# Optimization experiments

Hardware: AMD Instinct MI355X
Metric: run time of the kernel (lower is better)

## Reference

```python
import jax, jax.numpy as jnp
import numpy as np

B, N, D = 16, 4096, 64  # (batch*heads, seq_len, head_dim)

def setup_inputs() -> dict:
    key = jax.random.key(0)
    kq, kk, kv = jax.random.split(key, 3)
    queries = jax.random.normal(kq, (B, N, D), dtype=jnp.float32)
    keys = jax.random.normal(kk, (B, N, D), dtype=jnp.float32)
    values = jax.random.normal(kv, (B, N, D), dtype=jnp.float32)
    masking = jnp.zeros((B, N), dtype=jnp.float32)
    return {"queries": queries, "keys": keys, "values": values, "masking": masking}

def reference(queries, keys, values, masking):
    # Faithful to source: masks() computes the additive mask but returns
    # `inputs` unchanged (bug in original), so `masking` is a no-op.
    d = queries.shape[-1]
    scores = jnp.einsum('bnd,bmd->bnm', queries, keys) / jnp.sqrt(jnp.float32(d))
    attn = jax.nn.softmax(scores, axis=-1)
    # Dropout(rate=0) at inference is identity.
    out = jnp.einsum('bnm,bmd->bnd', attn, values)
    return out
```

## Files before the change

### kernel.cpp

```cpp
#include <hip/hip_runtime.h>
#include <hip/hip_bf16.h>

#define B_    16
#define N_    4096
#define D_    64
#define QBLK  128
#define KVBLK 64
#define KTILES (N_ / KVBLK)

typedef __attribute__((ext_vector_type(8))) short short8v;
typedef __attribute__((ext_vector_type(4))) float f32x4;
typedef __attribute__((ext_vector_type(4))) unsigned uint4v;

__device__ __forceinline__ short f2bf(float x) {
    union { float f; unsigned u; } c; c.f = x;
    unsigned r = c.u + 0x7FFFu + ((c.u >> 16) & 1u);
    return (short)(r >> 16);
}
__device__ __forceinline__ unsigned cvtpk(float lo, float hi) {
    unsigned r;
    asm("v_cvt_pk_bf16_f32 %0, %1, %2" : "=v"(r) : "v"(lo), "v"(hi));
    return r;
}
__device__ __forceinline__ float fexp2(float x) {
    float r;
    asm("v_exp_f32 %0, %1" : "=v"(r) : "v"(x));
    return r;
}

#define GLDS16(g, l)                                                      \
    __builtin_amdgcn_global_load_lds(                                     \
        (const __attribute__((address_space(1))) void*)(g),               \
        (__attribute__((address_space(3))) void*)(l), 16, 0, 0)

__global__ __launch_bounds__(256) void conv_k(const float* __restrict__ K,
                                              short* __restrict__ Kp) {
    const int idx  = blockIdx.x * 256 + threadIdx.x;
    const int nout = idx >> 3;
    const int c8   = (idx & 7) << 3;
    const int p    = nout & 63;
    const int sig  = (p & 3) | (((p >> 4) & 1) << 2) |
                     (((p >> 2) & 3) << 3) | ((p >> 5) << 5);
    const int nsrc = (nout & ~63) | sig;
    const float* src = K + (size_t)nsrc * D_ + c8;
    const f32x4 a = *(const f32x4*)src;
    const f32x4 b = *(const f32x4*)(src + 4);
    short8v o;
    o[0] = f2bf(a[0]); o[1] = f2bf(a[1]); o[2] = f2bf(a[2]); o[3] = f2bf(a[3]);
    o[4] = f2bf(b[0]); o[5] = f2bf(b[1]); o[6] = f2bf(b[2]); o[7] = f2bf(b[3]);
    const int cs = c8 ^ ((p & 7) << 3);
    *(short8v*)(Kp + (size_t)nout * D_ + cs) = o;
}

__global__ __launch_bounds__(256) void conv_v(const float* __restrict__ V,
                                              short* __restrict__ Vp) {
    __shared__ short Tl[64][68];
    const int b  = blockIdx.x >> 6;
    const int n0 = (blockIdx.x & 63) * 64;
    const int t  = threadIdx.x;
    const int r  = t >> 2;
    const int c0 = (t & 3) * 16;
    const float* src = V + ((size_t)b * N_ + n0 + r) * D_ + c0;
    const f32x4 v0 = *(const f32x4*)(src);
    const f32x4 v1 = *(const f32x4*)(src + 4);
    const f32x4 v2 = *(const f32x4*)(src + 8);
    const f32x4 v3 = *(const f32x4*)(src + 12);
    short8v lo, hi;
    lo[0]=f2bf(v0[0]); lo[1]=f2bf(v0[1]); lo[2]=f2bf(v0[2]); lo[3]=f2bf(v0[3]);
    lo[4]=f2bf(v1[0]); lo[5]=f2bf(v1[1]); lo[6]=f2bf(v1[2]); lo[7]=f2bf(v1[3]);
    hi[0]=f2bf(v2[0]); hi[1]=f2bf(v2[1]); hi[2]=f2bf(v2[2]); hi[3]=f2bf(v2[3]);
    hi[4]=f2bf(v3[0]); hi[5]=f2bf(v3[1]); hi[6]=f2bf(v3[2]); hi[7]=f2bf(v3[3]);
    *(short8v*)&Tl[r][c0]     = lo;
    *(short8v*)&Tl[r][c0 + 8] = hi;
    __syncthreads();
    const int d  = t >> 2;
    const int nb = (t & 3) * 16;
    const int s  = (d & 7) << 3;
    short8v o0, o1;
    #pragma unroll
    for (int j = 0; j < 8; ++j) {
        o0[j] = Tl[nb + j][d];
        o1[j] = Tl[nb + 8 + j][d];
    }
    short* dst = Vp + ((size_t)b * D_ + d) * N_ + n0;
    *(short8v*)(dst + (nb ^ s))       = o0;
    *(short8v*)(dst + ((nb + 8) ^ s)) = o1;
}

__global__ __launch_bounds__(256) void attn_fwd(
    const float* __restrict__ Qg, const short* __restrict__ Kp,
    const short* __restrict__ Vp, float* __restrict__ Og)
{
    __shared__ __align__(16) short Kl[4][KVBLK][D_];
    __shared__ __align__(16) short Vl[4][D_][KVBLK];

    const int tid  = threadIdx.x;
    const int w    = tid >> 6;
    const int lane = tid & 63;
    const int g    = lane >> 4;
    const int r16  = lane & 15;

    const int wg    = (blockIdx.x & 7) * 64 + (blockIdx.x >> 3);
    const int batch = wg >> 5;
    const int q0    = (wg & 31) * QBLK;

    const float SC = 0.18033688011112042f;
    const float* qrowA = Qg + ((size_t)batch * N_ + q0 + 32 * w + r16) * D_;
    const float* qrowB = qrowA + 16 * D_;
    short8v qfA[2], qfB[2];
    #pragma unroll
    for (int c = 0; c < 2; ++c) {
        const f32x4 a0 = *(const f32x4*)(qrowA + 32 * c + 8 * g);
        const f32x4 a1 = *(const f32x4*)(qrowA + 32 * c + 8 * g + 4);
        const f32x4 b0 = *(const f32x4*)(qrowB + 32 * c + 8 * g);
        const f32x4 b1 = *(const f32x4*)(qrowB + 32 * c + 8 * g + 4);
        short8v fa, fb;
        fa[0] = f2bf(a0[0] * SC); fa[1] = f2bf(a0[1] * SC);
        fa[2] = f2bf(a0[2] * SC); fa[3] = f2bf(a0[3] * SC);
        fa[4] = f2bf(a1[0] * SC); fa[5] = f2bf(a1[1] * SC);
        fa[6] = f2bf(a1[2] * SC); fa[7] = f2bf(a1[3] * SC);
        fb[0] = f2bf(b0[0] * SC); fb[1] = f2bf(b0[1] * SC);
        fb[2] = f2bf(b0[2] * SC); fb[3] = f2bf(b0[3] * SC);
        fb[4] = f2bf(b1[0] * SC); fb[5] = f2bf(b1[1] * SC);
        fb[6] = f2bf(b1[2] * SC); fb[7] = f2bf(b1[3] * SC);
        qfA[c] = fa;
        qfB[c] = fb;
    }

    f32x4 oA[4], oB[4];
    #pragma unroll
    for (int dt = 0; dt < 4; ++dt) {
        oA[dt] = (f32x4){0.f, 0.f, 0.f, 0.f};
        oB[dt] = (f32x4){0.f, 0.f, 0.f, 0.f};
    }
    float lA = 0.f, lB = 0.f;

    const short* kbase = Kp + (size_t)batch * N_ * D_;
    const short* vbase = Vp + (size_t)batch * D_ * (size_t)N_;
    const int    swz   = (r16 & 7) << 3;
    const int    vrow  = (lane >> 3);
    const int    vcol  = (lane & 7) * 8;

#define STAGE(bb, kt_)                                                        \
    {                                                                         \
        const int kv0_ = (kt_) * KVBLK;                                       \
        _Pragma("unroll")                                                     \
        for (int j = 0; j < 2; ++j) {                                         \
            const short* gk = kbase + (size_t)kv0_ * D_ + w * 1024 + j * 512 + lane * 8; \
            GLDS16(gk, (short*)Kl[bb] + w * 1024 + j * 512);                  \
            const int dr_ = w * 16 + j * 8 + vrow;                            \
            const short* gv = vbase + (size_t)dr_ * N_ + kv0_ + vcol;         \
            GLDS16(gv, (short*)Vl[bb] + w * 1024 + j * 512);                  \
        }                                                                     \
    }

#define COMPUTE(bb, kt_)                                                      \
    {                                                                         \
        f32x4 sA[4], sB[4];                                                   \
        _Pragma("unroll")                                                     \
        for (int n = 0; n < 4; ++n) {                                         \
            sA[n] = (f32x4){0.f, 0.f, 0.f, 0.f};                              \
            sB[n] = (f32x4){0.f, 0.f, 0.f, 0.f};                              \
        }                                                                     \
        __builtin_amdgcn_s_setprio(1);                                        \
        _Pragma("unroll")                                                     \
        for (int c = 0; c < 2; ++c) {                                         \
            _Pragma("unroll")                                                 \
            for (int n = 0; n < 4; ++n) {                                     \
                const short8v kf = *(const short8v*)                          \
                    &Kl[bb][r16 + 16 * n][(32 * c + 8 * g) ^ swz];            \
                sA[n] = __builtin_amdgcn_mfma_f32_16x16x32_bf16(              \
                    kf, qfA[c], sA[n], 0, 0, 0);                              \
                sB[n] = __builtin_amdgcn_mfma_f32_16x16x32_bf16(              \
                    kf, qfB[c], sB[n], 0, 0, 0);                              \
            }                                                                 \
        }                                                                     \
        __builtin_amdgcn_s_setprio(0);                                        \
        _Pragma("unroll")                                                     \
        for (int n = 0; n < 4; ++n) {                                         \
            _Pragma("unroll")                                                 \
            for (int i = 0; i < 4; ++i) {                                     \
                sA[n][i] = fexp2(sA[n][i]);                                   \
                sB[n][i] = fexp2(sB[n][i]);                                   \
            }                                                                 \
        }                                                                     \
        {                                                                     \
            float s0 = (sA[0][0] + sA[0][1]) + (sA[0][2] + sA[0][3]);         \
            float s1 = (sA[1][0] + sA[1][1]) + (sA[1][2] + sA[1][3]);         \
            float s2 = (sA[2][0] + sA[2][1]) + (sA[2][2] + sA[2][3]);         \
            float s3 = (sA[3][0] + sA[3][1]) + (sA[3][2] + sA[3][3]);         \
            lA += (s0 + s1) + (s2 + s3);                                      \
        }                                                                     \
        {                                                                     \
            float s0 = (sB[0][0] + sB[0][1]) + (sB[0][2] + sB[0][3]);         \
            float s1 = (sB[1][0] + sB[1][1]) + (sB[1][2] + sB[1][3]);         \
            float s2 = (sB[2][0] + sB[2][1]) + (sB[2][2] + sB[2][3]);         \
            float s3 = (sB[3][0] + sB[3][1]) + (sB[3][2] + sB[3][3]);         \
            lB += (s0 + s1) + (s2 + s3);                                      \
        }                                                                     \
        union { uint4v u; short8v v; } fA0, fA1, fB0, fB1;                    \
        fA0.u[0] = cvtpk(sA[0][0], sA[0][1]);                                 \
        fA0.u[1] = cvtpk(sA[0][2], sA[0][3]);                                 \
        fA0.u[2] = cvtpk(sA[1][0], sA[1][1]);                                 \
        fA0.u[3] = cvtpk(sA[1][2], sA[1][3]);                                 \
        fA1.u[0] = cvtpk(sA[2][0], sA[2][1]);                                 \
        fA1.u[1] = cvtpk(sA[2][2], sA[2][3]);                                 \
        fA1.u[2] = cvtpk(sA[3][0], sA[3][1]);                                 \
        fA1.u[3] = cvtpk(sA[3][2], sA[3][3]);                                 \
        fB0.u[0] = cvtpk(sB[0][0], sB[0][1]);                                 \
        fB0.u[1] = cvtpk(sB[0][2], sB[0][3]);                                 \
        fB0.u[2] = cvtpk(sB[1][0], sB[1][1]);                                 \
        fB0.u[3] = cvtpk(sB[1][2], sB[1][3]);                                 \
        fB1.u[0] = cvtpk(sB[2][0], sB[2][1]);                                 \
        fB1.u[1] = cvtpk(sB[2][2], sB[2][3]);                                 \
        fB1.u[2] = cvtpk(sB[3][0], sB[3][1]);                                 \
        fB1.u[3] = cvtpk(sB[3][2], sB[3][3]);                                 \
        __builtin_amdgcn_s_setprio(1);                                        \
        _Pragma("unroll")                                                     \
        for (int dt = 0; dt < 4; ++dt) {                                      \
            const short8v vf = *(const short8v*)                              \
                &Vl[bb][16 * dt + r16][(8 * g) ^ swz];                        \
            oA[dt] = __builtin_amdgcn_mfma_f32_16x16x32_bf16(                 \
                vf, fA0.v, oA[dt], 0, 0, 0);                                  \
            oB[dt] = __builtin_amdgcn_mfma_f32_16x16x32_bf16(                 \
                vf, fB0.v, oB[dt], 0, 0, 0);                                  \
        }                                                                     \
        _Pragma("unroll")                                                     \
        for (int dt = 0; dt < 4; ++dt) {                                      \
            const short8v vf = *(const short8v*)                              \
                &Vl[bb][16 * dt + r16][(32 + 8 * g) ^ swz];                   \
            oA[dt] = __builtin_amdgcn_mfma_f32_16x16x32_bf16(                 \
                vf, fA1.v, oA[dt], 0, 0, 0);                                  \
            oB[dt] = __builtin_amdgcn_mfma_f32_16x16x32_bf16(                 \
                vf, fB1.v, oB[dt], 0, 0, 0);                                  \
        }                                                                     \
        __builtin_amdgcn_s_setprio(0);                                        \
    }

    STAGE(0, 0);
    STAGE(1, 1);

    for (int kt = 0; kt < KTILES; kt += 2) {
        asm volatile("s_waitcnt vmcnt(0)" ::: "memory");
        __builtin_amdgcn_s_barrier();
        asm volatile("" ::: "memory");

        if (kt + 2 < KTILES) {
            STAGE((kt + 2) & 3, kt + 2);
            STAGE((kt + 3) & 3, kt + 3);
        }

        COMPUTE(kt & 3, kt);
        COMPUTE((kt + 1) & 3, kt + 1);
    }

    lA += __shfl_xor(lA, 16); lA += __shfl_xor(lA, 32);
    lB += __shfl_xor(lB, 16); lB += __shfl_xor(lB, 32);
    const float invA = 1.0f / lA;
    const float invB = 1.0f / lB;
    float* obA = Og + ((size_t)batch * N_ + q0 + 32 * w + r16) * D_;
    float* obB = obA + 16 * D_;
    #pragma unroll
    for (int dt = 0; dt < 4; ++dt) {
        f32x4 ra = oA[dt], rb = oB[dt];
        ra[0] *= invA; ra[1] *= invA; ra[2] *= invA; ra[3] *= invA;
        rb[0] *= invB; rb[1] *= invB; rb[2] *= invB; rb[3] *= invB;
        *(f32x4*)(obA + 16 * dt + 4 * g) = ra;
        *(f32x4*)(obB + 16 * dt + 4 * g) = rb;
    }
#undef STAGE
#undef COMPUTE
}

extern "C" void kernel_launch(void* const* d_in, const int* in_sizes, int n_in,
                              void* d_out, int out_size, void* d_ws, size_t ws_size,
                              hipStream_t stream) {
    const float* Qg = (const float*)d_in[0];
    const float* Kg = (const float*)d_in[1];
    const float* Vg = (const float*)d_in[2];
    float* Og = (float*)d_out;

    const size_t nelem = (size_t)B_ * N_ * D_;
    short* Kp = (short*)d_ws;
    short* Vp = Kp + nelem;

    conv_k<<<dim3(B_ * N_ * 8 / 256), dim3(256), 0, stream>>>(Kg, Kp);
    conv_v<<<dim3(B_ * (N_ / 64)), dim3(256), 0, stream>>>(Vg, Vp);
    attn_fwd<<<dim3(B_ * (N_ / QBLK)), dim3(256), 0, stream>>>(Qg, Kp, Vp, Og);
}
```

Before: 96.37 us.

## Load V fragments directly from global into registers, double-buffered across tiles

V tiles are no longer staged through LDS. Each wave loads its V MFMA operands straight from global memory into registers one tile ahead, using two alternating register sets. The freed LDS doubles the K ring to 8 buffers, so the loop now stages and processes 4 tiles per barrier instead of 2. The V transpose kernel drops its XOR swizzle to match, and the first QK MFMA now takes a zero constant instead of zeroed accumulators. This raises register pressure and relies on uncoalesced-ish global/L2 reads for V. The blocking vmcnt(0) wait at each barrier may also stall on the outstanding V loads.

```diff
diff --git a/kernel.cpp b/kernel.cpp
--- a/kernel.cpp
+++ b/kernel.cpp
@@ -75,7 +75,6 @@
     __syncthreads();
     const int d  = t >> 2;
     const int nb = (t & 3) * 16;
-    const int s  = (d & 7) << 3;
     short8v o0, o1;
     #pragma unroll
     for (int j = 0; j < 8; ++j) {
@@ -83,16 +82,15 @@
         o1[j] = Tl[nb + 8 + j][d];
     }
     short* dst = Vp + ((size_t)b * D_ + d) * N_ + n0;
-    *(short8v*)(dst + (nb ^ s))       = o0;
-    *(short8v*)(dst + ((nb + 8) ^ s)) = o1;
+    *(short8v*)(dst + nb)     = o0;
+    *(short8v*)(dst + nb + 8) = o1;
 }
 
 __global__ __launch_bounds__(256) void attn_fwd(
     const float* __restrict__ Qg, const short* __restrict__ Kp,
     const short* __restrict__ Vp, float* __restrict__ Og)
 {
-    __shared__ __align__(16) short Kl[4][KVBLK][D_];
-    __shared__ __align__(16) short Vl[4][D_][KVBLK];
+    __shared__ __align__(16) short Kl[8][KVBLK][D_];
 
     const int tid  = threadIdx.x;
     const int w    = tid >> 6;
@@ -134,12 +132,11 @@
         oB[dt] = (f32x4){0.f, 0.f, 0.f, 0.f};
     }
     float lA = 0.f, lB = 0.f;
+    const f32x4 Z4 = (f32x4){0.f, 0.f, 0.f, 0.f};
 
     const short* kbase = Kp + (size_t)batch * N_ * D_;
     const short* vbase = Vp + (size_t)batch * D_ * (size_t)N_;
     const int    swz   = (r16 & 7) << 3;
-    const int    vrow  = (lane >> 3);
-    const int    vcol  = (lane & 7) * 8;
 
 #define STAGE(bb, kt_)                                                        \
     {                                                                         \
@@ -148,32 +145,42 @@
         for (int j = 0; j < 2; ++j) {                                         \
             const short* gk = kbase + (size_t)kv0_ * D_ + w * 1024 + j * 512 + lane * 8; \
             GLDS16(gk, (short*)Kl[bb] + w * 1024 + j * 512);                  \
-            const int dr_ = w * 16 + j * 8 + vrow;                            \
-            const short* gv = vbase + (size_t)dr_ * N_ + kv0_ + vcol;         \
-            GLDS16(gv, (short*)Vl[bb] + w * 1024 + j * 512);                  \
-        }                                                                     \
-    }
-
-#define COMPUTE(bb, kt_)                                                      \
+        }                                                                     \
+    }
+
+#define LOADV(V_, kt_)                                                        \
     {                                                                         \
+        const int ktc_ = (kt_) < KTILES ? (kt_) : KTILES - 1;                 \
+        const short* vp_ = vbase + ktc_ * KVBLK;                              \
+        _Pragma("unroll")                                                     \
+        for (int dt = 0; dt < 4; ++dt) {                                      \
+            V_[2*dt]   = *(const short8v*)(vp_ + (size_t)(16*dt + r16) * N_ + 8*g);      \
+            V_[2*dt+1] = *(const short8v*)(vp_ + (size_t)(16*dt + r16) * N_ + 8*g + 32); \
+        }                                                                     \
+    }
+
+#define COMPUTE(bb, VU, VI, ktn)                                              \
+    {                                                                         \
+        LOADV(VI, ktn);                                                       \
         f32x4 sA[4], sB[4];                                                   \
+        __builtin_amdgcn_s_setprio(1);                                        \
         _Pragma("unroll")                                                     \
         for (int n = 0; n < 4; ++n) {                                         \
-            sA[n] = (f32x4){0.f, 0.f, 0.f, 0.f};                              \
-            sB[n] = (f32x4){0.f, 0.f, 0.f, 0.f};                              \
-        }                                                                     \
-        __builtin_amdgcn_s_setprio(1);                                        \
-        _Pragma("unroll")                                                     \
-        for (int c = 0; c < 2; ++c) {                                         \
-            _Pragma("unroll")                                                 \
-            for (int n = 0; n < 4; ++n) {                                     \
-                const short8v kf = *(const short8v*)                          \
-                    &Kl[bb][r16 + 16 * n][(32 * c + 8 * g) ^ swz];            \
-                sA[n] = __builtin_amdgcn_mfma_f32_16x16x32_bf16(              \
-                    kf, qfA[c], sA[n], 0, 0, 0);                              \
-                sB[n] = __builtin_amdgcn_mfma_f32_16x16x32_bf16(              \
-                    kf, qfB[c], sB[n], 0, 0, 0);                              \
-            }                                                                 \
+            const short8v kf0 = *(const short8v*)                             \
+                &Kl[bb][r16 + 16 * n][(8 * g) ^ swz];                         \
+            sA[n] = __builtin_amdgcn_mfma_f32_16x16x32_bf16(                  \
+                kf0, qfA[0], Z4, 0, 0, 0);                                    \
+            sB[n] = __builtin_amdgcn_mfma_f32_16x16x32_bf16(                  \
+                kf0, qfB[0], Z4, 0, 0, 0);                                    \
+        }                                                                     \
+        _Pragma("unroll")                                                     \
+        for (int n = 0; n < 4; ++n) {                                         \
+            const short8v kf1 = *(const short8v*)                             \
+                &Kl[bb][r16 + 16 * n][(32 + 8 * g) ^ swz];                    \
+            sA[n] = __builtin_amdgcn_mfma_f32_16x16x32_bf16(                  \
+                kf1, qfA[1], sA[n], 0, 0, 0);                                 \
+            sB[n] = __builtin_amdgcn_mfma_f32_16x16x32_bf16(                  \
+                kf1, qfB[1], sB[n], 0, 0, 0);                                 \
         }                                                                     \
         __builtin_amdgcn_s_setprio(0);                                        \
         _Pragma("unroll")                                                     \
@@ -218,40 +225,41 @@
         __builtin_amdgcn_s_setprio(1);                                        \
         _Pragma("unroll")                                                     \
         for (int dt = 0; dt < 4; ++dt) {                                      \
-            const short8v vf = *(const short8v*)                              \
-                &Vl[bb][16 * dt + r16][(8 * g) ^ swz];                        \
             oA[dt] = __builtin_amdgcn_mfma_f32_16x16x32_bf16(                 \
-                vf, fA0.v, oA[dt], 0, 0, 0);                                  \
+                VU[2*dt], fA0.v, oA[dt], 0, 0, 0);                            \
             oB[dt] = __builtin_amdgcn_mfma_f32_16x16x32_bf16(                 \
-                vf, fB0.v, oB[dt], 0, 0, 0);                                  \
+                VU[2*dt], fB0.v, oB[dt], 0, 0, 0);                            \
         }                                                                     \
         _Pragma("unroll")                                                     \
         for (int dt = 0; dt < 4; ++dt) {                                      \
-            const short8v vf = *(const short8v*)                              \
-                &Vl[bb][16 * dt + r16][(32 + 8 * g) ^ swz];                   \
             oA[dt] = __builtin_amdgcn_mfma_f32_16x16x32_bf16(                 \
-                vf, fA1.v, oA[dt], 0, 0, 0);                                  \
+                VU[2*dt+1], fA1.v, oA[dt], 0, 0, 0);                          \
             oB[dt] = __builtin_amdgcn_mfma_f32_16x16x32_bf16(                 \
-                vf, fB1.v, oB[dt], 0, 0, 0);                                  \
+                VU[2*dt+1], fB1.v, oB[dt], 0, 0, 0);                          \
         }                                                                     \
         __builtin_amdgcn_s_setprio(0);                                        \
     }
 
-    STAGE(0, 0);
-    STAGE(1, 1);
-
-    for (int kt = 0; kt < KTILES; kt += 2) {
+    short8v vA[8], vB[8];
+    STAGE(0, 0); STAGE(1, 1); STAGE(2, 2); STAGE(3, 3);
+    LOADV(vA, 0);
+
+    for (int kt = 0; kt < KTILES; kt += 4) {
         asm volatile("s_waitcnt vmcnt(0)" ::: "memory");
         __builtin_amdgcn_s_barrier();
         asm volatile("" ::: "memory");
 
-        if (kt + 2 < KTILES) {
-            STAGE((kt + 2) & 3, kt + 2);
-            STAGE((kt + 3) & 3, kt + 3);
+        if (kt + 4 < KTILES) {
+            STAGE((kt + 4) & 7, kt + 4);
+            STAGE((kt + 5) & 7, kt + 5);
+            STAGE((kt + 6) & 7, kt + 6);
+            STAGE((kt + 7) & 7, kt + 7);
         }
 
-        COMPUTE(kt & 3, kt);
-        COMPUTE((kt + 1) & 3, kt + 1);
+        COMPUTE( kt      & 7, vA, vB, kt + 1);
+        COMPUTE((kt + 1) & 7, vB, vA, kt + 2);
+        COMPUTE((kt + 2) & 7, vA, vB, kt + 3);
+        COMPUTE((kt + 3) & 7, vB, vA, kt + 4);
     }
 
     lA += __shfl_xor(lA, 16); lA += __shfl_xor(lA, 32);
@@ -269,6 +277,7 @@
         *(f32x4*)(obB + 16 * dt + 4 * g) = rb;
     }
 #undef STAGE
+#undef LOADV
 #undef COMPUTE
 }
 
```

Result: slower. 159.4 us (+65.4%).
